# Performance work log

Hardware: AMD Instinct MI355X
Metric: run time of the kernel (lower is better)

## Reference

```python
import jax, jax.numpy as jnp
import numpy as np

B = 100000   # batch of nodes
K = 10       # sampled neighbours per node
N = 1000000  # total nodes in feature table
D = 128      # feature dim


def setup_inputs() -> dict:
    key = jax.random.key(0)
    k1, k2, k3 = jax.random.split(key, 3)
    nodes = jax.random.randint(k1, (B,), 0, N, dtype=jnp.int64)
    neighbours = jax.random.randint(k2, (B, K), 0, N, dtype=jnp.int64)
    features = jax.random.normal(k3, (N, D), dtype=jnp.float32)
    return {"nodes": nodes, "neighbours": neighbours, "features": features}


def reference(nodes, neighbours, features):
    # Neighborhood = sampled neighbours union self node -> [B, K+1]
    neigh_idx = jnp.concatenate([neighbours, nodes[:, None]], axis=1)
    # Gather features: [B, K+1, D] (irregular memory-bound gather)
    gathered = features[neigh_idx]
    # Row-normalized mask matmul == mean over the neighborhood axis
    return gathered.mean(axis=1)  # [B, D]
```

## Files before the change

### kernel.cpp

```cpp
#include <hip/hip_runtime.h>


#define KNEIGH 10
#define DDIM 128

__global__ __launch_bounds__(256) void MeanAggregator_36386962932386_kernel(
    const int* __restrict__ nodes,
    const int* __restrict__ neighbours,
    const float* __restrict__ features,
    float* __restrict__ out,
    int B)
{
    const int node = blockIdx.x * 4 + (threadIdx.x >> 6);
    if (node >= B) return;
    const int lane = threadIdx.x & 63;

    int idx[KNEIGH + 1];
    const long long nb = (long long)node * KNEIGH;
#pragma unroll
    for (int j = 0; j < KNEIGH; ++j) idx[j] = neighbours[nb + j];
    idx[KNEIGH] = nodes[node];

    float2 v[KNEIGH + 1];
#pragma unroll
    for (int j = 0; j < KNEIGH + 1; ++j) {
        const float2* row = (const float2*)(features + (long long)idx[j] * DDIM);
        v[j] = row[lane];
    }

    float2 acc = v[0];
#pragma unroll
    for (int j = 1; j < KNEIGH + 1; ++j) {
        acc.x += v[j].x;
        acc.y += v[j].y;
    }

    const float s = 1.0f / (float)(KNEIGH + 1);
    float2 o;
    o.x = acc.x * s;
    o.y = acc.y * s;
    ((float2*)(out + (long long)node * DDIM))[lane] = o;
}

extern "C" void kernel_launch(void* const* d_in, const int* in_sizes, int n_in,
                              void* d_out, int out_size, void* d_ws, size_t ws_size,
                              hipStream_t stream)
{
    const int* nodes      = (const int*)d_in[0];
    const int* neighbours = (const int*)d_in[1];
    const float* features = (const float*)d_in[2];
    float* out            = (float*)d_out;

    const int B = in_sizes[0];
    const int blocks = (B + 3) / 4;

    MeanAggregator_36386962932386_kernel<<<blocks, 256, 0, stream>>>(
        nodes, neighbours, features, out, B);
}
```

Baseline: 652.0 us.

## Process two nodes per wave with 16-byte loads and grid-stride index prefetch

Each wavefront now handles two nodes, one per 32-lane half, and each lane loads float4 instead of float2, so every row gather is a 16-byte vector access. The kernel becomes a persistent grid-stride loop capped at 2048 blocks, with the next pair's neighbour indices prefetched while the current row gathers are in flight. Neighbour indices are read as int2 pairs, offsets use 32-bit arithmetic, and outputs use nontemporal stores. The 32-bit offsets assume the feature table stays under 4 GiB, and the block cap could reduce memory-level parallelism.

Result: no change. 654.1 us (+0.3%).

```diff
diff --git a/kernel.cpp b/kernel.cpp
--- a/kernel.cpp
+++ b/kernel.cpp
@@ -3,6 +3,8 @@
 
 #define KNEIGH 10
 #define DDIM 128
+
+typedef float v4f __attribute__((ext_vector_type(4)));
 
 __global__ __launch_bounds__(256) void MeanAggregator_36386962932386_kernel(
     const int* __restrict__ nodes,
@@ -11,35 +13,75 @@
     float* __restrict__ out,
     int B)
 {
-    const int node = blockIdx.x * 4 + (threadIdx.x >> 6);
-    if (node >= B) return;
+    const int wave = blockIdx.x * 4 + (threadIdx.x >> 6);
     const int lane = threadIdx.x & 63;
+    const int half = lane >> 5;
+    const int hl   = lane & 31;
+    const unsigned hb = (unsigned)hl * 16u;
+
+    const int npairs = (B + 1) >> 1;
+    const int nwaves = gridDim.x * 4;
+
+    int pair = wave;
+    if (pair >= npairs) return;
 
     int idx[KNEIGH + 1];
-    const long long nb = (long long)node * KNEIGH;
+    int node;
+
+    {
+        node = pair * 2 + half;
+        const int n = node < B ? node : 0;
+        const int2* p2 = (const int2*)((const char*)neighbours + (unsigned)n * (KNEIGH * 4));
 #pragma unroll
-    for (int j = 0; j < KNEIGH; ++j) idx[j] = neighbours[nb + j];
-    idx[KNEIGH] = nodes[node];
-
-    float2 v[KNEIGH + 1];
-#pragma unroll
-    for (int j = 0; j < KNEIGH + 1; ++j) {
-        const float2* row = (const float2*)(features + (long long)idx[j] * DDIM);
-        v[j] = row[lane];
+        for (int j = 0; j < KNEIGH / 2; ++j) {
+            const int2 t = p2[j];
+            idx[2 * j]     = t.x;
+            idx[2 * j + 1] = t.y;
+        }
+        idx[KNEIGH] = nodes[n];
     }
 
-    float2 acc = v[0];
+    while (true) {
+        v4f v[KNEIGH + 1];
 #pragma unroll
-    for (int j = 1; j < KNEIGH + 1; ++j) {
-        acc.x += v[j].x;
-        acc.y += v[j].y;
+        for (int j = 0; j < KNEIGH + 1; ++j) {
+            const unsigned off = (unsigned)idx[j] * (DDIM * 4) + hb;
+            v[j] = *(const v4f*)((const char*)features + off);
+        }
+
+        const int next = pair + nwaves;
+        const bool have_next = next < npairs;
+        int nidx[KNEIGH + 1];
+        int nnode = 0;
+        if (have_next) {
+            nnode = next * 2 + half;
+            const int n = nnode < B ? nnode : 0;
+            const int2* p2 = (const int2*)((const char*)neighbours + (unsigned)n * (KNEIGH * 4));
+#pragma unroll
+            for (int j = 0; j < KNEIGH / 2; ++j) {
+                const int2 t = p2[j];
+                nidx[2 * j]     = t.x;
+                nidx[2 * j + 1] = t.y;
+            }
+            nidx[KNEIGH] = nodes[n];
+        }
+
+        v4f acc = v[0];
+#pragma unroll
+        for (int j = 1; j < KNEIGH + 1; ++j) acc += v[j];
+        acc *= (1.0f / (KNEIGH + 1));
+
+        if (node < B) {
+            const unsigned ooff = (unsigned)node * (DDIM * 4) + hb;
+            __builtin_nontemporal_store(acc, (v4f*)((char*)out + ooff));
+        }
+
+        if (!have_next) break;
+        pair = next;
+        node = nnode;
+#pragma unroll
+        for (int j = 0; j < KNEIGH + 1; ++j) idx[j] = nidx[j];
     }
-
-    const float s = 1.0f / (float)(KNEIGH + 1);
-    float2 o;
-    o.x = acc.x * s;
-    o.y = acc.y * s;
-    ((float2*)(out + (long long)node * DDIM))[lane] = o;
 }
 
 extern "C" void kernel_launch(void* const* d_in, const int* in_sizes, int n_in,
@@ -52,7 +94,9 @@
     float* out            = (float*)d_out;
 
     const int B = in_sizes[0];
-    const int blocks = (B + 3) / 4;
+    const int npairs = (B + 1) / 2;
+    int blocks = (npairs + 3) / 4;
+    if (blocks > 2048) blocks = 2048;
 
     MeanAggregator_36386962932386_kernel<<<blocks, 256, 0, stream>>>(
         nodes, neighbours, features, out, B);
```
